# Kernel tuning notes

Measured on AMD Instinct MI355X. Metric: run time of the kernel, lower is better.

The kernel has to match this reference:

```python
import jax, jax.numpy as jnp
import numpy as np

EPS = 1.0 / 137.0  # fine-structure-constant epsilon used throughout the Yat ops


def yat_dense(x, W, b, alpha):
    # x: [..., C], W: [C, F] -> [..., F]
    dot = jnp.einsum('btc,cf->btf', x, W)
    x_norm = jnp.sum(x * x, axis=-1, keepdims=True)        # [..., 1]
    w_norm = jnp.sum(W * W, axis=0)                         # [F]
    dist = x_norm + w_norm - 2.0 * dot
    y = dot * dot / (dist + EPS)
    y = y + b
    F = W.shape[1]
    scale = (np.sqrt(F) / np.log(1.0 + F)) ** 1.0           # base; alpha exponent applied below
    return y * ((np.float32(np.sqrt(F)) / np.float32(np.log1p(F))) ** alpha)


def setup_inputs() -> dict:
    key = jax.random.key(0)
    ks = jax.random.split(key, 8)
    B, T, C = 4, 1024, 768
    x = jax.random.normal(ks[0], (B, T, C), dtype=jnp.float32)
    mask = jnp.tril(jnp.ones((T, T), dtype=bool))[None, None, :, :]  # causal [1,1,T,T]
    sd = 1.0 / np.sqrt(C)
    W_attn = jax.random.normal(ks[1], (C, 3 * C), dtype=jnp.float32) * sd
    b_attn = jnp.zeros((3 * C,), dtype=jnp.float32)
    alpha_attn = jnp.ones((), dtype=jnp.float32)
    W_proj = jax.random.normal(ks[2], (C, C), dtype=jnp.float32) * sd
    b_proj = jnp.zeros((C,), dtype=jnp.float32)
    alpha_proj = jnp.ones((), dtype=jnp.float32)
    return {"x": x, "mask": mask, "W_attn": W_attn, "b_attn": b_attn,
            "alpha_attn": alpha_attn, "W_proj": W_proj, "b_proj": b_proj,
            "alpha_proj": alpha_proj}


def reference(x, mask, W_attn, b_attn, alpha_attn, W_proj, b_proj, alpha_proj):
    B, T, C = x.shape
    H = 12
    D = C // H  # head_dim
    qkv = yat_dense(x, W_attn, b_attn, alpha_attn)          # [B,T,3C]
    qkv = qkv.reshape(B, T, 3 * H, D)
    q, k, v = jnp.array_split(qkv, 3, axis=2)
    q = jnp.transpose(q, (0, 2, 1, 3))                       # [B,H,T,D]
    k = jnp.transpose(k, (0, 2, 1, 3))
    v = jnp.transpose(v, (0, 2, 1, 3))
    scale = 1.0 / np.float32(np.sqrt(D))
    dot = jnp.einsum('bhid,bhjd->bhij', q, k)                # [B,H,T,T]
    sq_dot = jnp.square(dot * scale)
    q_norm = jnp.sum(jnp.square(q), axis=-1)[..., None]      # [B,H,T,1]
    k_norm = jnp.sum(jnp.square(k), axis=-1)[..., None, :]   # [B,H,1,T]
    sq_dist = q_norm + k_norm - 2.0 * dot * scale
    attn = sq_dot / (sq_dist + EPS)
    attn = jnp.where(mask, attn, jnp.finfo(jnp.float32).min)
    attn = jax.nn.softmax(attn, axis=-1)
    out = jnp.einsum('bhij,bhjd->bhid', attn, v)             # [B,H,T,D]
    out = jnp.transpose(out, (0, 2, 1, 3)).reshape(B, T, C)
    out = yat_dense(out, W_proj, b_proj, alpha_proj)         # [B,T,C]
    return out
```

## Files before the change

kernel.cpp:

```cpp
#include <hip/hip_runtime.h>
#include <math.h>

#define EPS_YAT (1.0f/137.0f)

typedef unsigned short u16;
typedef unsigned int u32;
typedef __attribute__((ext_vector_type(8))) __bf16 bf16x8;
typedef __attribute__((ext_vector_type(4))) float f32x4;

__device__ __forceinline__ float4 ld4(const float* p) { return *(const float4*)p; }

__device__ __forceinline__ u16 bf16_rne(float f) {
    u32 u = __float_as_uint(f);
    u32 r = (u + 0x7fffu + ((u >> 16) & 1u)) >> 16;
    return (u16)r;
}
__device__ __forceinline__ float bf16_f(u16 h) {
    return __uint_as_float(((u32)h) << 16);
}

__device__ __forceinline__ void glds16(const u16* g, u16* s) {
    __builtin_amdgcn_global_load_lds(
        (const __attribute__((address_space(1))) void*)g,
        (__attribute__((address_space(3))) void*)s,
        16, 0, 0);
}

__global__ void colnorm_part(const float* __restrict__ W, float* __restrict__ part,
                             int K, int N) {
    __shared__ float sm[256];
    const int col = blockIdx.x * 64 + (threadIdx.x & 63);
    const int q = threadIdx.x >> 6;
    const int rows = K >> 6;
    const int k0 = blockIdx.y * (K >> 4) + q * rows;
    float s = 0.f;
    for (int k = k0; k < k0 + rows; ++k) {
        float w = W[(size_t)k * N + col];
        s += w * w;
    }
    sm[threadIdx.x] = s;
    __syncthreads();
    if (threadIdx.x < 64)
        part[(size_t)blockIdx.y * N + col] =
            sm[threadIdx.x] + sm[threadIdx.x + 64] + sm[threadIdx.x + 128] + sm[threadIdx.x + 192];
}

__global__ void colnorm_reduce(const float* __restrict__ part, float* __restrict__ wn,
                               int N) {
    int gid = blockIdx.x * 256 + threadIdx.x;
    if (gid >= N) return;
    float s = 0.f;
    #pragma unroll
    for (int i = 0; i < 16; ++i) s += part[(size_t)i * N + gid];
    wn[gid] = s;
}

__global__ void rownorm_kernel(const float* __restrict__ X, float* __restrict__ rn, int K) {
    int wave = threadIdx.x >> 6;
    int lane = threadIdx.x & 63;
    int row = blockIdx.x * 4 + wave;
    const float* xr = X + (size_t)row * K;
    float s = 0.f;
    for (int k = lane * 4; k < K; k += 256) {
        float4 v = ld4(xr + k);
        s += v.x * v.x + v.y * v.y + v.z * v.z + v.w * v.w;
    }
    for (int off = 32; off; off >>= 1) s += __shfl_down(s, off);
    if (lane == 0) rn[row] = s;
}

__global__ void rownorm_hl(const u16* __restrict__ Xh, const u16* __restrict__ Xl,
                           float* __restrict__ rn) {
    int wave = threadIdx.x >> 6;
    int lane = threadIdx.x & 63;
    int row = blockIdx.x * 4 + wave;
    const u16* xh = Xh + (size_t)row * 768;
    const u16* xl = Xl + (size_t)row * 768;
    float s = 0.f;
    for (int k = lane * 4; k < 768; k += 256) {
        uint2 hv = *(const uint2*)(xh + k);
        uint2 lv = *(const uint2*)(xl + k);
        float a0 = bf16_f((u16)hv.x)         + bf16_f((u16)lv.x);
        float a1 = bf16_f((u16)(hv.x >> 16)) + bf16_f((u16)(lv.x >> 16));
        float a2 = bf16_f((u16)hv.y)         + bf16_f((u16)lv.y);
        float a3 = bf16_f((u16)(hv.y >> 16)) + bf16_f((u16)(lv.y >> 16));
        s += a0 * a0 + a1 * a1 + a2 * a2 + a3 * a3;
    }
    for (int off = 32; off; off >>= 1) s += __shfl_down(s, off);
    if (lane == 0) rn[row] = s;
}

__global__ void qknorm_kernel(const u16* __restrict__ qh, const u16* __restrict__ ql,
                              float* __restrict__ qn, float* __restrict__ kn) {
    int gid = blockIdx.x * 256 + threadIdx.x;
    int lane = gid & 15;
    int idx = gid >> 4;
    int which = (idx >= 49152) ? 1 : 0;
    int r = idx - which * 49152;
    int t = r & 1023;
    int bh = r >> 10;
    int h = bh % 12, b = bh / 12;
    const size_t off = (size_t)(b * 1024 + t) * 2304 + which * 768 + h * 64 + lane * 4;
    uint2 hv = *(const uint2*)(qh + off);
    uint2 lv = *(const uint2*)(ql + off);
    float a0 = bf16_f((u16)hv.x)         + bf16_f((u16)lv.x);
    float a1 = bf16_f((u16)(hv.x >> 16)) + bf16_f((u16)(lv.x >> 16));
    float a2 = bf16_f((u16)hv.y)         + bf16_f((u16)lv.y);
    float a3 = bf16_f((u16)(hv.y >> 16)) + bf16_f((u16)(lv.y >> 16));
    float s = a0 * a0 + a1 * a1 + a2 * a2 + a3 * a3;
    s += __shfl_xor(s, 1, 16);
    s += __shfl_xor(s, 2, 16);
    s += __shfl_xor(s, 4, 16);
    s += __shfl_xor(s, 8, 16);
    if (lane == 0) (which ? kn : qn)[r] = s;
}

__global__ void split_kernel(const float* __restrict__ X, u16* __restrict__ Xh,
                             u16* __restrict__ Xl, int n4) {
    int gid = blockIdx.x * 256 + threadIdx.x;
    if (gid >= n4) return;
    float4 v = ld4(X + (size_t)gid * 4);
    u16 h0 = bf16_rne(v.x), h1 = bf16_rne(v.y), h2 = bf16_rne(v.z), h3 = bf16_rne(v.w);
    u16 l0 = bf16_rne(v.x - bf16_f(h0));
    u16 l1 = bf16_rne(v.y - bf16_f(h1));
    u16 l2 = bf16_rne(v.z - bf16_f(h2));
    u16 l3 = bf16_rne(v.w - bf16_f(h3));
    uint2 hp, lp;
    hp.x = (u32)h0 | ((u32)h1 << 16); hp.y = (u32)h2 | ((u32)h3 << 16);
    lp.x = (u32)l0 | ((u32)l1 << 16); lp.y = (u32)l2 | ((u32)l3 << 16);
    *(uint2*)(Xh + (size_t)gid * 4) = hp;
    *(uint2*)(Xl + (size_t)gid * 4) = lp;
}

__global__ void split_wt_kernel(const float* __restrict__ W, u16* __restrict__ Th,
                                u16* __restrict__ Tl, int K, int N) {
    __shared__ float tile[64 * 68];
    const int tid = threadIdx.x;
    const int n0 = blockIdx.x << 6;
    const int k0 = blockIdx.y << 6;
    const int rr = tid >> 4;
    const int cc = (tid & 15) << 2;
    #pragma unroll
    for (int s = 0; s < 4; ++s) {
        int k_l = rr + s * 16;
        *(float4*)&tile[k_l * 68 + cc] = ld4(W + (size_t)(k0 + k_l) * N + n0 + cc);
    }
    __syncthreads();
    #pragma unroll
    for (int s = 0; s < 4; ++s) {
        int n_l = rr + s * 16;
        float a0 = tile[(cc + 0) * 68 + n_l];
        float a1 = tile[(cc + 1) * 68 + n_l];
        float a2 = tile[(cc + 2) * 68 + n_l];
        float a3 = tile[(cc + 3) * 68 + n_l];
        u16 h0 = bf16_rne(a0), h1 = bf16_rne(a1), h2 = bf16_rne(a2), h3 = bf16_rne(a3);
        u16 l0 = bf16_rne(a0 - bf16_f(h0));
        u16 l1 = bf16_rne(a1 - bf16_f(h1));
        u16 l2 = bf16_rne(a2 - bf16_f(h2));
        u16 l3 = bf16_rne(a3 - bf16_f(h3));
        uint2 hp, lp;
        hp.x = (u32)h0 | ((u32)h1 << 16); hp.y = (u32)h2 | ((u32)h3 << 16);
        lp.x = (u32)l0 | ((u32)l1 << 16); lp.y = (u32)l2 | ((u32)l3 << 16);
        size_t o = (size_t)(n0 + n_l) * K + k0 + cc;
        *(uint2*)(Th + o) = hp;
        *(uint2*)(Tl + o) = lp;
    }
}

template<int SPLIT, int NB>
__global__ __launch_bounds__(256, 4)
void yat_gemm_mfma(const u16* __restrict__ Ah, const u16* __restrict__ Al,
                   const u16* __restrict__ Bh, const u16* __restrict__ Bl,
                   const float* __restrict__ bias, const float* __restrict__ xn,
                   const float* __restrict__ wnc, const float* __restrict__ alphap,
                   const float Fdim, float* __restrict__ out,
                   u16* __restrict__ outh, u16* __restrict__ outl,
                   const int N, const int K) {
    __shared__ __align__(16) u16 lds[4096 + NB * 4096];
    const int tid = threadIdx.x;
    const int m0 = blockIdx.y << 6;
    const int n0 = blockIdx.x * (64 * NB);
    const int w = tid >> 6;
    const int l = tid & 63;
    const int lm = l & 15;
    const int kq = l >> 4;
    const int kq4 = kq << 2;
    const int wn = w * 16 * NB;

    const int srow = (w << 4) + (l >> 2);
    const int scol = (l & 3) << 3;
    const u16* gA  = Ah + (size_t)(m0 + srow) * K + scol;
    const u16* gC  = Al + (size_t)(m0 + srow) * K + scol;
    const u16* gB  = Bh + (size_t)(n0 + srow) * K + scol;
    const u16* gD  = Bl + (size_t)(n0 + srow) * K + scol;
    const u16* gB2 = Bh + (size_t)(n0 + 64 + srow) * K + scol;
    const u16* gD2 = Bl + (size_t)(n0 + 64 + srow) * K + scol;
    const int wb = w << 9;

    u16* sAh = lds;
    u16* sAl = lds + 2048;
    u16* sBh = lds + 4096;
    u16* sBl = lds + 4096 + 2048 * NB;

    f32x4 acc[4][NB] = {};

    for (int k0 = 0; k0 < K; k0 += 32) {
        __syncthreads();
        glds16(gA + k0, sAh + wb);
        glds16(gC + k0, sAl + wb);
        glds16(gB + k0, sBh + wb);
        glds16(gD + k0, sBl + wb);
        if constexpr (NB == 2) {
            glds16(gB2 + k0, sBh + 2048 + wb);
            glds16(gD2 + k0, sBl + 2048 + wb);
        }
        __syncthreads();

        bf16x8 fah[4], fal[4], fbh[NB], fbl[NB];
        #pragma unroll
        for (int i = 0; i < 4; ++i) {
            const int ra = (i * 16 + lm) * 32 + (kq << 3);
            fah[i] = *(const bf16x8*)&sAh[ra];
            fal[i] = *(const bf16x8*)&sAl[ra];
        }
        #pragma unroll
        for (int j = 0; j < NB; ++j) {
            const int rb = (wn + j * 16 + lm) * 32 + (kq << 3);
            fbh[j] = *(const bf16x8*)&sBh[rb];
            fbl[j] = *(const bf16x8*)&sBl[rb];
        }
        #pragma unroll
        for (int i = 0; i < 4; ++i)
            #pragma unroll
            for (int j = 0; j < NB; ++j) {
                f32x4 c = acc[i][j];
                c = __builtin_amdgcn_mfma_f32_16x16x32_bf16(fah[i], fbh[j], c, 0, 0, 0);
                c = __builtin_amdgcn_mfma_f32_16x16x32_bf16(fah[i], fbl[j], c, 0, 0, 0);
                c = __builtin_amdgcn_mfma_f32_16x16x32_bf16(fal[i], fbh[j], c, 0, 0, 0);
                acc[i][j] = c;
            }
    }

    const float scale = powf(sqrtf(Fdim) / log1pf(Fdim), *alphap);
    #pragma unroll
    for (int i = 0; i < 4; ++i) {
        const int mbase = m0 + i * 16 + kq4;
        #pragma unroll
        for (int j = 0; j < NB; ++j) {
            const int n = n0 + wn + j * 16 + lm;
            const float w2 = wnc[n];
            const float bv = bias[n];
            #pragma unroll
            for (int r = 0; r < 4; ++r) {
                const int m = mbase + r;
                float d = acc[i][j][r];
                float den = xn[m] + w2 - 2.f * d + EPS_YAT;
                float v = (d * d / den + bv) * scale;
                if constexpr (SPLIT) {
                    u16 hh = bf16_rne(v);
                    outh[(size_t)m * N + n] = hh;
                    outl[(size_t)m * N + n] = bf16_rne(v - bf16_f(hh));
                } else {
                    out[(size_t)m * N + n] = v;
                }
            }
        }
    }
}

#define MFMA_B16(a, b, c) __builtin_amdgcn_mfma_f32_16x16x32_bf16(a, b, c, 0, 0, 0)

#define ST_TILE(j) { \
    const int kro = ((j)*16 + lm) * 72 + (kq << 3); \
    bf16x8 kh = *(const bf16x8*)&KPh[kro]; \
    bf16x8 kl = *(const bf16x8*)&KPl[kro]; \
    st##j = MFMA_B16(kh, qh0, st##j); \
    st##j = MFMA_B16(kl, qh0, st##j); \
    st##j = MFMA_B16(kh, ql0, st##j); \
    kh = *(const bf16x8*)&KPh[kro + 32]; \
    kl = *(const bf16x8*)&KPl[kro + 32]; \
    st##j = MFMA_B16(kh, qh1, st##j); \
    st##j = MFMA_B16(kl, qh1, st##j); \
    st##j = MFMA_B16(kh, ql1, st##j); \
}

#define YAT_EL(j, r) { \
    float sv = st##j[r] * 0.125f; \
    float den = qnm + kns[(j)*16 + kq4 + (r)] - 2.f * sv + EPS_YAT; \
    float v = sv * sv / den; \
    if (diag && ((j)*16 + kq4 + (r) > wband + lm)) v = -3e38f; \
    st##j[r] = v; mm = fmaxf(mm, v); }
#define YAT_TILE(j) YAT_EL(j,0) YAT_EL(j,1) YAT_EL(j,2) YAT_EL(j,3)

#define PEXP_TILE(j) { \
    float p0 = __expf(st##j[0] - mnew), p1 = __expf(st##j[1] - mnew); \
    float p2 = __expf(st##j[2] - mnew), p3 = __expf(st##j[3] - mnew); \
    rs += p0 + p1 + p2 + p3; \
    u16 h0 = bf16_rne(p0), h1 = bf16_rne(p1), h2 = bf16_rne(p2), h3 = bf16_rne(p3); \
    uint2 hp; hp.x = (u32)h0 | ((u32)h1 << 16); hp.y = (u32)h2 | ((u32)h3 << 16); \
    *(uint2*)&KPh[pmrow + (j)*16 + kq4] = hp; \
    u16 e0 = bf16_rne(p0 - bf16_f(h0)), e1 = bf16_rne(p1 - bf16_f(h1)); \
    u16 e2 = bf16_rne(p2 - bf16_f(h2)), e3 = bf16_rne(p3 - bf16_f(h3)); \
    uint2 lp; lp.x = (u32)e0 | ((u32)e1 << 16); lp.y = (u32)e2 | ((u32)e3 << 16); \
    *(uint2*)&KPl[pmrow + (j)*16 + kq4] = lp; }

#define PV_TILE(j) { \
    const int vro = ((j)*16 + lm) * 72 + vkq8; \
    bf16x8 vh = *(const bf16x8*)&Vth[vro]; \
    bf16x8 vl = *(const bf16x8*)&Vtl[vro]; \
    ac##j = MFMA_B16(ph0, vh, ac##j); \
    ac##j = MFMA_B16(pl0, vh, ac##j); \
    ac##j = MFMA_B16(ph0, vl, ac##j); \
    vh = *(const bf16x8*)&Vth[vro + 32]; \
    vl = *(const bf16x8*)&Vtl[vro + 32]; \
    ac##j = MFMA_B16(ph1, vh, ac##j); \
    ac##j = MFMA_B16(pl1, vh, ac##j); \
    ac##j = MFMA_B16(ph1, vl, ac##j); \
}

#define WRVT(dst, v2, m) { \
    dst[(sj * 4 + 16 * (m) + 0) * 72 + toks] = (u16)((v2).x); \
    dst[(sj * 4 + 16 * (m) + 1) * 72 + toks] = (u16)((v2).x >> 16); \
    dst[(sj * 4 + 16 * (m) + 2) * 72 + toks] = (u16)((v2).y); \
    dst[(sj * 4 + 16 * (m) + 3) * 72 + toks] = (u16)((v2).y >> 16); }

__global__ __launch_bounds__(256, 4)
void yat_flash_mfma(const u16* __restrict__ qh_g, const u16* __restrict__ ql_g,
                    const float* __restrict__ qn, const float* __restrict__ kn,
                    u16* __restrict__ outh, u16* __restrict__ outl) {
    __shared__ __align__(16) u16 KPh[64 * 72], KPl[64 * 72];
    __shared__ __align__(16) u16 Vth[64 * 72], Vtl[64 * 72];
    __shared__ float kns[64];

    const int tid = threadIdx.x;
    const int L = blockIdx.x;
    const int u = L / 48;
    const int qt = (u & 1) ? (u >> 1) : (15 - (u >> 1));
    const int bh = L % 48;
    const int h = bh % 12, b = bh / 12;
    const int wave = tid >> 6;
    const int lane = tid & 63;
    const int lm = lane & 15;
    const int kq = lane >> 4;
    const int kq4 = kq << 2;
    const int wband = wave << 4;
    const int sr = tid >> 2;
    const int sj = tid & 3;
    const int toks = sr ^ (sj << 3);
    const int vkq8 = (kq ^ (lm >> 2)) << 3;
    const size_t base = (size_t)(b * 1024) * 2304 + h * 64;

    {
        const size_t qoff = base + (size_t)((qt << 6) + sr) * 2304 + sj * 16;
        *(uint4*)&KPh[sr * 72 + sj * 16]     = *(const uint4*)(qh_g + qoff);
        *(uint4*)&KPh[sr * 72 + sj * 16 + 8] = *(const uint4*)(qh_g + qoff + 8);
        *(uint4*)&KPl[sr * 72 + sj * 16]     = *(const uint4*)(ql_g + qoff);
        *(uint4*)&KPl[sr * 72 + sj * 16 + 8] = *(const uint4*)(ql_g + qoff + 8);
    }
    const float qnm = qn[bh * 1024 + (qt << 6) + wband + lm];

    const size_t r0 = base + (size_t)sr * 2304;
    uint4 kh0 = *(const uint4*)(qh_g + r0 + 768 + sj * 16);
    uint4 kh1 = *(const uint4*)(qh_g + r0 + 768 + sj * 16 + 8);
    uint4 kl0 = *(const uint4*)(ql_g + r0 + 768 + sj * 16);
    uint4 kl1 = *(const uint4*)(ql_g + r0 + 768 + sj * 16 + 8);
    uint2 vh0 = *(const uint2*)(qh_g + r0 + 1536 + sj * 4);
    uint2 vh1 = *(const uint2*)(qh_g + r0 + 1536 + sj * 4 + 16);
    uint2 vh2 = *(const uint2*)(qh_g + r0 + 1536 + sj * 4 + 32);
    uint2 vh3 = *(const uint2*)(qh_g + r0 + 1536 + sj * 4 + 48);
    uint2 vl0 = *(const uint2*)(ql_g + r0 + 1536 + sj * 4);
    uint2 vl1 = *(const uint2*)(ql_g + r0 + 1536 + sj * 4 + 16);
    uint2 vl2 = *(const uint2*)(ql_g + r0 + 1536 + sj * 4 + 32);
    uint2 vl3 = *(const uint2*)(ql_g + r0 + 1536 + sj * 4 + 48);
    float knS = (tid < 64) ? kn[bh * 1024 + tid] : 0.f;

    __syncthreads();

    const int qrow = (wband + lm) * 72;
    const bf16x8 qh0 = *(const bf16x8*)&KPh[qrow + (kq << 3)];
    const bf16x8 qh1 = *(const bf16x8*)&KPh[qrow + 32 + (kq << 3)];
    const bf16x8 ql0 = *(const bf16x8*)&KPl[qrow + (kq << 3)];
    const bf16x8 ql1 = *(const bf16x8*)&KPl[qrow + 32 + (kq << 3)];

    f32x4 ac0 = {}, ac1 = {}, ac2 = {}, ac3 = {};
    float mrun = -3e38f, lrun = 0.f;
    const int pmrow = (wband + lm) * 72;

    for (int kt = 0; kt <= qt; ++kt) {
        __syncthreads();
        *(uint4*)&KPh[sr * 72 + sj * 16]     = kh0;
        *(uint4*)&KPh[sr * 72 + sj * 16 + 8] = kh1;
        *(uint4*)&KPl[sr * 72 + sj * 16]     = kl0;
        *(uint4*)&KPl[sr * 72 + sj * 16 + 8] = kl1;
        WRVT(Vth, vh0, 0) WRVT(Vth, vh1, 1) WRVT(Vth, vh2, 2) WRVT(Vth, vh3, 3)
        WRVT(Vtl, vl0, 0) WRVT(Vtl, vl1, 1) WRVT(Vtl, vl2, 2) WRVT(Vtl, vl3, 3)
        if (tid < 64) kns[tid] = knS;
        __syncthreads();

        if (kt < qt) {
            const size_t r = base + (size_t)(((kt + 1) << 6) + sr) * 2304;
            kh0 = *(const uint4*)(qh_g + r + 768 + sj * 16);
            kh1 = *(const uint4*)(qh_g + r + 768 + sj * 16 + 8);
            kl0 = *(const uint4*)(ql_g + r + 768 + sj * 16);
            kl1 = *(const uint4*)(ql_g + r + 768 + sj * 16 + 8);
            vh0 = *(const uint2*)(qh_g + r + 1536 + sj * 4);
            vh1 = *(const uint2*)(qh_g + r + 1536 + sj * 4 + 16);
            vh2 = *(const uint2*)(qh_g + r + 1536 + sj * 4 + 32);
            vh3 = *(const uint2*)(qh_g + r + 1536 + sj * 4 + 48);
            vl0 = *(const uint2*)(ql_g + r + 1536 + sj * 4);
            vl1 = *(const uint2*)(ql_g + r + 1536 + sj * 4 + 16);
            vl2 = *(const uint2*)(ql_g + r + 1536 + sj * 4 + 32);
            vl3 = *(const uint2*)(ql_g + r + 1536 + sj * 4 + 48);
            if (tid < 64) knS = kn[bh * 1024 + ((kt + 1) << 6) + tid];
        }

        f32x4 st0 = {}, st1 = {}, st2 = {}, st3 = {};
        __builtin_amdgcn_s_setprio(1);
        ST_TILE(0) ST_TILE(1) ST_TILE(2) ST_TILE(3)
        __builtin_amdgcn_s_setprio(0);
        __syncthreads();

        const bool diag = (kt == qt);
        float mm = -3e38f;
        YAT_TILE(0) YAT_TILE(1) YAT_TILE(2) YAT_TILE(3)
        mm = fmaxf(mm, __shfl_xor(mm, 16));
        mm = fmaxf(mm, __shfl_xor(mm, 32));
        const float mnew = fmaxf(mrun, mm);
        const float al = __expf(mrun - mnew);
        mrun = mnew;
        float rs = 0.f;
        PEXP_TILE(0) PEXP_TILE(1) PEXP_TILE(2) PEXP_TILE(3)
        rs += __shfl_xor(rs, 16);
        rs += __shfl_xor(rs, 32);
        lrun = lrun * al + rs;
        const float a0 = __shfl(al, kq4 + 0, 16);
        const float a1 = __shfl(al, kq4 + 1, 16);
        const float a2 = __shfl(al, kq4 + 2, 16);
        const float a3 = __shfl(al, kq4 + 3, 16);
        ac0[0] *= a0; ac0[1] *= a1; ac0[2] *= a2; ac0[3] *= a3;
        ac1[0] *= a0; ac1[1] *= a1; ac1[2] *= a2; ac1[3] *= a3;
        ac2[0] *= a0; ac2[1] *= a1; ac2[2] *= a2; ac2[3] *= a3;
        ac3[0] *= a0; ac3[1] *= a1; ac3[2] *= a2; ac3[3] *= a3;
        __syncthreads();

        const bf16x8 ph0 = *(const bf16x8*)&KPh[pmrow + (kq << 3)];
        const bf16x8 ph1 = *(const bf16x8*)&KPh[pmrow + 32 + (kq << 3)];
        const bf16x8 pl0 = *(const bf16x8*)&KPl[pmrow + (kq << 3)];
        const bf16x8 pl1 = *(const bf16x8*)&KPl[pmrow + 32 + (kq << 3)];
        __builtin_amdgcn_s_setprio(1);
        PV_TILE(0) PV_TILE(1) PV_TILE(2) PV_TILE(3)
        __builtin_amdgcn_s_setprio(0);
    }

    const float i0 = 1.f / __shfl(lrun, kq4 + 0, 16);
    const float i1 = 1.f / __shfl(lrun, kq4 + 1, 16);
    const float i2 = 1.f / __shfl(lrun, kq4 + 2, 16);
    const float i3 = 1.f / __shfl(lrun, kq4 + 3, 16);
    const size_t obase = (size_t)(b * 1024 + (qt << 6) + wband + kq4) * 768 + h * 64 + lm;
    u16* oph = outh + obase;
    u16* opl = outl + obase;
    #define STORE_E(j, r, iv) { \
        float ov = ac##j[r] * iv; \
        u16 hh = bf16_rne(ov); \
        oph[(size_t)(r) * 768 + (j)*16] = hh; \
        opl[(size_t)(r) * 768 + (j)*16] = bf16_rne(ov - bf16_f(hh)); }
    #define STORE_T(j) { STORE_E(j,0,i0) STORE_E(j,1,i1) STORE_E(j,2,i2) STORE_E(j,3,i3) }
    STORE_T(0) STORE_T(1) STORE_T(2) STORE_T(3)
    #undef STORE_T
    #undef STORE_E
}

extern "C" void kernel_launch(void* const* d_in, const int* in_sizes, int n_in,
                              void* d_out, int out_size, void* d_ws, size_t ws_size,
                              hipStream_t stream) {
    const float* x          = (const float*)d_in[0];
    const float* W_attn     = (const float*)d_in[2];
    const float* b_attn     = (const float*)d_in[3];
    const float* alpha_attn = (const float*)d_in[4];
    const float* W_proj     = (const float*)d_in[5];
    const float* b_proj     = (const float*)d_in[6];
    const float* alpha_proj = (const float*)d_in[7];

    float* ws       = (float*)d_ws;
    u16*   qkvh     = (u16*)ws;
    u16*   qkvl     = (u16*)(ws + 4718592);
    float* xn       = ws + 12582912;
    float* an       = ws + 12587008;
    float* wn_attn  = ws + 12591104;
    float* wn_proj  = ws + 12593408;
    float* qn       = ws + 12594176;
    float* kn       = ws + 12643328;

    float* cn_part_a = ws + 9437184;
    float* cn_part_p = ws + 9437184 + 36864;
    u16* xh  = (u16*)(ws + 9437184);
    u16* xl  = (u16*)(ws + 11010048);
    u16* aoh = (u16*)(ws + 9437184);
    u16* aol = (u16*)(ws + 11010048);
    u16* wth = (u16*)d_out;
    u16* wtl = (u16*)d_out + 1769472;
    u16* wph = (u16*)(ws + 3145728);
    u16* wpl = (u16*)(ws + 3440640);

    colnorm_part<<<dim3(36, 16), 256, 0, stream>>>(W_attn, cn_part_a, 768, 2304);
    colnorm_part<<<dim3(12, 16), 256, 0, stream>>>(W_proj, cn_part_p, 768, 768);
    colnorm_reduce<<<9, 256, 0, stream>>>(cn_part_a, wn_attn, 2304);
    colnorm_reduce<<<3, 256, 0, stream>>>(cn_part_p, wn_proj, 768);
    rownorm_kernel<<<1024, 256, 0, stream>>>(x, xn, 768);
    split_kernel<<<3072, 256, 0, stream>>>(x, xh, xl, 786432);
    split_wt_kernel<<<dim3(36, 12), 256, 0, stream>>>(W_attn, wth, wtl, 768, 2304);
    yat_gemm_mfma<1, 2><<<dim3(18, 64), 256, 0, stream>>>(
        xh, xl, wth, wtl, b_attn, xn, wn_attn, alpha_attn, 2304.f,
        nullptr, qkvh, qkvl, 2304, 768);
    qknorm_kernel<<<6144, 256, 0, stream>>>(qkvh, qkvl, qn, kn);
    yat_flash_mfma<<<768, 256, 0, stream>>>(qkvh, qkvl, qn, kn, aoh, aol);
    rownorm_hl<<<1024, 256, 0, stream>>>(aoh, aol, an);
    split_wt_kernel<<<dim3(12, 12), 256, 0, stream>>>(W_proj, wph, wpl, 768, 768);
    yat_gemm_mfma<0, 1><<<dim3(12, 64), 256, 0, stream>>>(
        aoh, aol, wph, wpl, b_proj, an, wn_proj, alpha_proj, 768.f,
        (float*)d_out, nullptr, nullptr, 768, 768);
}
```

Measured before the change: 270.6 us.

## Fuse x split with row norm, swizzle GEMM blocks, relax flash launch bounds

Merges the row-norm and bf16 hi/lo split of x into a single kernel, so x is read once and one launch is dropped. Remaps GEMM workgroup indices with an interleaving swizzle to change the order tiles are visited, aiming at better cache reuse of the A/B operands. Lowers the flash-attention launch-bounds occupancy hint from 4 to 2 so the compiler has more registers per thread, at the cost of fewer resident waves.

After: 259.2 us. -4.2%, faster.

```diff
diff --git a/kernel.cpp b/kernel.cpp
--- a/kernel.cpp
+++ b/kernel.cpp
@@ -55,15 +55,29 @@
     wn[gid] = s;
 }
 
-__global__ void rownorm_kernel(const float* __restrict__ X, float* __restrict__ rn, int K) {
+__global__ void split_rownorm(const float* __restrict__ X, u16* __restrict__ Xh,
+                              u16* __restrict__ Xl, float* __restrict__ rn) {
     int wave = threadIdx.x >> 6;
     int lane = threadIdx.x & 63;
     int row = blockIdx.x * 4 + wave;
-    const float* xr = X + (size_t)row * K;
+    const float* xr = X + (size_t)row * 768;
+    u16* xh = Xh + (size_t)row * 768;
+    u16* xl = Xl + (size_t)row * 768;
     float s = 0.f;
-    for (int k = lane * 4; k < K; k += 256) {
+    #pragma unroll
+    for (int k = lane * 4; k < 768; k += 256) {
         float4 v = ld4(xr + k);
         s += v.x * v.x + v.y * v.y + v.z * v.z + v.w * v.w;
+        u16 h0 = bf16_rne(v.x), h1 = bf16_rne(v.y), h2 = bf16_rne(v.z), h3 = bf16_rne(v.w);
+        u16 l0 = bf16_rne(v.x - bf16_f(h0));
+        u16 l1 = bf16_rne(v.y - bf16_f(h1));
+        u16 l2 = bf16_rne(v.z - bf16_f(h2));
+        u16 l3 = bf16_rne(v.w - bf16_f(h3));
+        uint2 hp, lp;
+        hp.x = (u32)h0 | ((u32)h1 << 16); hp.y = (u32)h2 | ((u32)h3 << 16);
+        lp.x = (u32)l0 | ((u32)l1 << 16); lp.y = (u32)l2 | ((u32)l3 << 16);
+        *(uint2*)(xh + k) = hp;
+        *(uint2*)(xl + k) = lp;
     }
     for (int off = 32; off; off >>= 1) s += __shfl_down(s, off);
     if (lane == 0) rn[row] = s;
@@ -115,23 +129,6 @@
     if (lane == 0) (which ? kn : qn)[r] = s;
 }
 
-__global__ void split_kernel(const float* __restrict__ X, u16* __restrict__ Xh,
-                             u16* __restrict__ Xl, int n4) {
-    int gid = blockIdx.x * 256 + threadIdx.x;
-    if (gid >= n4) return;
-    float4 v = ld4(X + (size_t)gid * 4);
-    u16 h0 = bf16_rne(v.x), h1 = bf16_rne(v.y), h2 = bf16_rne(v.z), h3 = bf16_rne(v.w);
-    u16 l0 = bf16_rne(v.x - bf16_f(h0));
-    u16 l1 = bf16_rne(v.y - bf16_f(h1));
-    u16 l2 = bf16_rne(v.z - bf16_f(h2));
-    u16 l3 = bf16_rne(v.w - bf16_f(h3));
-    uint2 hp, lp;
-    hp.x = (u32)h0 | ((u32)h1 << 16); hp.y = (u32)h2 | ((u32)h3 << 16);
-    lp.x = (u32)l0 | ((u32)l1 << 16); lp.y = (u32)l2 | ((u32)l3 << 16);
-    *(uint2*)(Xh + (size_t)gid * 4) = hp;
-    *(uint2*)(Xl + (size_t)gid * 4) = lp;
-}
-
 __global__ void split_wt_kernel(const float* __restrict__ W, u16* __restrict__ Th,
                                 u16* __restrict__ Tl, int K, int N) {
     __shared__ float tile[64 * 68];
@@ -178,8 +175,11 @@
                    const int N, const int K) {
     __shared__ __align__(16) u16 lds[4096 + NB * 4096];
     const int tid = threadIdx.x;
-    const int m0 = blockIdx.y << 6;
-    const int n0 = blockIdx.x * (64 * NB);
+    const int nwg = gridDim.x * gridDim.y;
+    const int orig = blockIdx.y * gridDim.x + blockIdx.x;
+    const int swz = (orig & 7) * (nwg >> 3) + (orig >> 3);
+    const int m0 = (swz / gridDim.x) << 6;
+    const int n0 = (swz % gridDim.x) * (64 * NB);
     const int w = tid >> 6;
     const int l = tid & 63;
     const int lm = l & 15;
@@ -324,7 +324,7 @@
     dst[(sj * 4 + 16 * (m) + 2) * 72 + toks] = (u16)((v2).y); \
     dst[(sj * 4 + 16 * (m) + 3) * 72 + toks] = (u16)((v2).y >> 16); }
 
-__global__ __launch_bounds__(256, 4)
+__global__ __launch_bounds__(256, 2)
 void yat_flash_mfma(const u16* __restrict__ qh_g, const u16* __restrict__ ql_g,
                     const float* __restrict__ qn, const float* __restrict__ kn,
                     u16* __restrict__ outh, u16* __restrict__ outl) {
@@ -506,8 +506,7 @@
     colnorm_part<<<dim3(12, 16), 256, 0, stream>>>(W_proj, cn_part_p, 768, 768);
     colnorm_reduce<<<9, 256, 0, stream>>>(cn_part_a, wn_attn, 2304);
     colnorm_reduce<<<3, 256, 0, stream>>>(cn_part_p, wn_proj, 768);
-    rownorm_kernel<<<1024, 256, 0, stream>>>(x, xn, 768);
-    split_kernel<<<3072, 256, 0, stream>>>(x, xh, xl, 786432);
+    split_rownorm<<<1024, 256, 0, stream>>>(x, xh, xl, xn);
     split_wt_kernel<<<dim3(36, 12), 256, 0, stream>>>(W_attn, wth, wtl, 768, 2304);
     yat_gemm_mfma<1, 2><<<dim3(18, 64), 256, 0, stream>>>(
         xh, xl, wth, wtl, b_attn, xn, wn_attn, alpha_attn, 2304.f,
```
